# Performance work log

Measured on AMD Instinct MI355X. Metric: run time of the kernel, lower is better.

Reference implementation:

```python
import jax, jax.numpy as jnp
import numpy as np
from math import factorial, sqrt

LMAX = 2
NB = 32
NRBF = 20
CUTOFF = 5.0
N_ATOMS = 20000
N_EDGES = 400000
T = 2
M = (LMAX + 1) ** 2
LIDX = np.repeat(np.arange(LMAX + 1), 2 * np.arange(LMAX + 1) + 1)  # l of each flat (l,m) index


def _cg_complex(j1, m1, j2, m2, j3, m3):
    # Racah formula for complex-SH Clebsch-Gordan coefficients
    if m3 != m1 + m2 or j3 < abs(j1 - j2) or j3 > j1 + j2:
        return 0.0
    f = factorial
    pref = sqrt((2 * j3 + 1) * f(j1 + j2 - j3) * f(j1 - j2 + j3) * f(-j1 + j2 + j3) / f(j1 + j2 + j3 + 1))
    pref *= sqrt(f(j1 + m1) * f(j1 - m1) * f(j2 + m2) * f(j2 - m2) * f(j3 + m3) * f(j3 - m3))
    kmin = max(0, j2 - j3 - m1, j1 + m2 - j3)
    kmax = min(j1 + j2 - j3, j1 - m1, j2 + m2)
    s = 0.0
    for k in range(kmin, kmax + 1):
        s += (-1) ** k / (f(k) * f(j1 + j2 - j3 - k) * f(j1 - m1 - k) * f(j2 + m2 - k) * f(j3 - j2 + m1 + k) * f(j3 - j1 - m2 + k))
    return pref * s


def _u_matrix(l):
    # real-SH = U @ complex-SH (rows: real m from -l..l, cols: complex m')
    U = np.zeros((2 * l + 1, 2 * l + 1), dtype=np.complex128)
    for m in range(-l, l + 1):
        if m == 0:
            U[l, l] = 1.0
        elif m > 0:
            U[l + m, l + m] = (-1) ** m / sqrt(2)
            U[l + m, l - m] = 1.0 / sqrt(2)
        else:
            mu = -m
            U[l + m, l + m] = 1j / sqrt(2)
            U[l + m, l - m] = -1j * (-1) ** mu / sqrt(2)
    return U


def _build_cg_rsh(lmax):
    # CG coefficients in the real-SH basis, parity invariant (odd l1+l2+l3 blocks zero)
    cg = np.zeros((M, M, M), dtype=np.float64)
    Us = [_u_matrix(l) for l in range(lmax + 1)]
    for l1 in range(lmax + 1):
        for l2 in range(lmax + 1):
            for l3 in range(lmax + 1):
                if (l1 + l2 + l3) % 2 == 1 or l3 < abs(l1 - l2) or l3 > l1 + l2:
                    continue
                Cc = np.zeros((2 * l1 + 1, 2 * l2 + 1, 2 * l3 + 1), dtype=np.complex128)
                for i, m1 in enumerate(range(-l1, l1 + 1)):
                    for j, m2 in enumerate(range(-l2, l2 + 1)):
                        m3 = m1 + m2
                        if abs(m3) <= l3:
                            Cc[i, j, l3 + m3] = _cg_complex(l1, m1, l2, m2, l3, m3)
                R = np.einsum('ai,bj,ck,ijk->abc', Us[l1], Us[l2], np.conj(Us[l3]), Cc)
                cg[l1 * l1:(l1 + 1) ** 2, l2 * l2:(l2 + 1) ** 2, l3 * l3:(l3 + 1) ** 2] = np.real(R)
    return cg.astype(np.float32)


CG = jnp.asarray(_build_cg_rsh(LMAX))   # [9, 9, 9]
LIDX_J = jnp.asarray(LIDX)


def _rsh(dirs):
    # real spherical harmonics up to l=2 on unit vectors, flat (l,m) order -> [P, 9]
    x, y, z = dirs[:, 0], dirs[:, 1], dirs[:, 2]
    c1 = 0.4886025119029199
    c2 = 1.0925484305920792
    return jnp.stack([
        jnp.full_like(x, 0.28209479177387814),
        c1 * y, c1 * z, c1 * x,
        c2 * x * y, c2 * y * z,
        0.31539156525252005 * (3.0 * z * z - 1.0),
        c2 * x * z,
        0.5462742152960396 * (x * x - y * y),
    ], axis=1)


def _forward(atomic_numbers, r_ij, idx_i, idx_j, emb, Wf, bf, Wm1, Wm2, Wm3, Wg, bg):
    d = jnp.linalg.norm(r_ij, axis=1)                      # [P]
    Y = _rsh(r_ij / d[:, None])                            # [P, 9]
    offsets = jnp.linspace(0.0, CUTOFF, NRBF)
    width = CUTOFF / (NRBF - 1)
    radial = jnp.exp(-0.5 / width ** 2 * (d[:, None] - offsets) ** 2)   # GaussianRBF [P, NRBF]
    fcut = jnp.where(d < CUTOFF, 0.5 * (jnp.cos(d * jnp.pi / CUTOFF) + 1.0), 0.0)  # CosineCutoff
    x0 = emb[atomic_numbers]                               # nuclear embedding [N, NB]
    x = jnp.concatenate([x0[:, None, :], jnp.zeros((x0.shape[0], M - 1, NB), x0.dtype)], axis=1)  # scalar2rsh
    for t in range(T):
        # SO3Convolution: per-edge radial filter per output degree l, cutoff gated
        Wl = ((radial @ Wf[t].T + bf[t]) * fcut[:, None]).reshape(-1, LMAX + 1, NB)
        xj = x[idx_j]                                      # gather neighbors [P, 9, NB]
        tbc = jnp.einsum('pa,abc->pbc', Y, CG)             # contract Y_ij with CG
        yij = jnp.einsum('pbc,pbn->pcn', tbc, xj) * Wl[:, LIDX_J, :]
        dx = jax.ops.segment_sum(yij, idx_i, num_segments=x.shape[0], indices_are_sorted=True)
        ddx = jnp.einsum('xcn,kn->xck', dx, Wm1[t])        # mixing1 (no bias)
        dx = dx + jnp.einsum('abc,xan,xbn->xcn', CG, dx, ddx)  # SO3TensorProduct
        dx = jnp.einsum('xcn,kn->xck', dx, Wm2[t])         # mixing2
        h = jax.nn.sigmoid((dx[:, 0, :] @ Wg[t].T + bg[t]).reshape(-1, LMAX + 1, NB))
        dx = dx * h[:, LIDX_J, :]                          # SO3ParametricGatedNonlinearity
        dx = jnp.einsum('xcn,kn->xck', dx, Wm3[t])         # mixing3
        x = x + dx
    return x                                               # multipole representation [N, 9, NB]


def setup_inputs():
    key = jax.random.key(0)
    ks = jax.random.split(key, 12)
    return {
        'atomic_numbers': jax.random.randint(ks[0], (N_ATOMS,), 1, 100),
        'r_ij': jax.random.normal(ks[1], (N_EDGES, 3), jnp.float32),
        'idx_i': jnp.sort(jax.random.randint(ks[2], (N_EDGES,), 0, N_ATOMS)),
        'idx_j': jax.random.randint(ks[3], (N_EDGES,), 0, N_ATOMS),
        'emb': jax.random.normal(ks[4], (101, NB), jnp.float32).at[0].set(0.0),
        'Wf': jax.random.normal(ks[5], (T, (LMAX + 1) * NB, NRBF), jnp.float32) / sqrt(NRBF),
        'bf': jnp.zeros((T, (LMAX + 1) * NB), jnp.float32),
        'Wm1': jax.random.normal(ks[6], (T, NB, NB), jnp.float32) / sqrt(NB),
        'Wm2': jax.random.normal(ks[7], (T, NB, NB), jnp.float32) / sqrt(NB),
        'Wm3': jax.random.normal(ks[8], (T, NB, NB), jnp.float32) / sqrt(NB),
        'Wg': jax.random.normal(ks[9], (T, (LMAX + 1) * NB, NB), jnp.float32) / sqrt(NB),
        'bg': jnp.zeros((T, (LMAX + 1) * NB), jnp.float32),
    }


def reference(atomic_numbers, r_ij, idx_i, idx_j, emb, Wf, bf, Wm1, Wm2, Wm3, Wg, bg):
    return _forward(atomic_numbers, r_ij, idx_i, idx_j, emb, Wf, bf, Wm1, Wm2, Wm3, Wg, bg)
```

## Files before the change

### kernel.cpp

```cpp
#include <hip/hip_runtime.h>

#define CHUNK 16

constexpr double CFACT[8] = {1.,1.,2.,6.,24.,120.,720.,5040.};

constexpr double csqrt(double x){
  if (x <= 0.0) return 0.0;
  double s = 1.0;
  while (x > 4.0)  { x *= 0.25; s *= 2.0; }
  while (x < 0.25) { x *= 4.0;  s *= 0.5; }
  double g = 1.0;
  for (int i=0;i<10;i++) g = 0.5*(g + x/g);
  return s*g;
}

constexpr double cg_complex(int j1,int m1,int j2,int m2,int j3,int m3){
  if (m3 != m1+m2 || j3 < (j1>j2?j1-j2:j2-j1) || j3 > j1+j2) return 0.0;
  double pref = csqrt((2.0*j3+1.0)*CFACT[j1+j2-j3]*CFACT[j1-j2+j3]*CFACT[-j1+j2+j3]/CFACT[j1+j2+j3+1]);
  pref *= csqrt(CFACT[j1+m1]*CFACT[j1-m1]*CFACT[j2+m2]*CFACT[j2-m2]*CFACT[j3+m3]*CFACT[j3-m3]);
  int kmin = 0;
  if (j2-j3-m1 > kmin) kmin = j2-j3-m1;
  if (j1+m2-j3 > kmin) kmin = j1+m2-j3;
  int kmax = j1+j2-j3;
  if (j1-m1 < kmax) kmax = j1-m1;
  if (j2+m2 < kmax) kmax = j2+m2;
  double s = 0.0;
  for (int k=kmin;k<=kmax;++k){
    double t = 1.0/(CFACT[k]*CFACT[j1+j2-j3-k]*CFACT[j1-m1-k]*CFACT[j2+m2-k]*CFACT[j3-j2+m1+k]*CFACT[j3-j1-m2+k]);
    s += (k&1)? -t : t;
  }
  return pref*s;
}

struct UR { int n; int mc[2]; double re[2]; double im[2]; };
constexpr UR u_row(int m){
  UR u{}; const double is2 = 0.70710678118654752440;
  if (m==0){ u.n=1; u.mc[0]=0; u.re[0]=1.0; u.im[0]=0.0; u.mc[1]=0; u.re[1]=0.0; u.im[1]=0.0; }
  else if (m>0){ u.n=2; u.mc[0]=m;  u.re[0]=((m&1)? -is2:is2); u.im[0]=0.0;
                        u.mc[1]=-m; u.re[1]=is2;               u.im[1]=0.0; }
  else { int mu=-m; u.n=2; u.mc[0]=m;  u.re[0]=0.0; u.im[0]=is2;
                           u.mc[1]=mu; u.re[1]=0.0; u.im[1]=((mu&1)? is2:-is2); }
  return u;
}

struct CGTab { float v[9][9][9]; };
constexpr CGTab build_cg(){
  CGTab g{};
  double cc[9][9][9] = {};
  for (int a=0;a<9;a++){
    int l1 = (a==0)?0:((a<4)?1:2); int m1 = a - (l1*l1+l1);
    for (int b=0;b<9;b++){
      int l2 = (b==0)?0:((b<4)?1:2); int m2 = b - (l2*l2+l2);
      int m3 = m1+m2;
      for (int l3=0;l3<=2;l3++){
        if (m3 < -l3 || m3 > l3) continue;
        cc[a][b][l3*l3+l3+m3] = cg_complex(l1,m1,l2,m2,l3,m3);
      }
    }
  }
  for (int l1=0;l1<=2;l1++) for (int l2=0;l2<=2;l2++) for (int l3=0;l3<=2;l3++){
    if (((l1+l2+l3)&1)==1) continue;
    int dl = (l1>l2)?(l1-l2):(l2-l1);
    if (l3 < dl || l3 > l1+l2) continue;
    for (int m1=-l1;m1<=l1;m1++) for (int m2=-l2;m2<=l2;m2++) for (int m3=-l3;m3<=l3;m3++){
      UR ua = u_row(m1), ub = u_row(m2), uc = u_row(m3);
      double acc = 0.0;
      for (int i=0;i<ua.n;i++) for (int j=0;j<ub.n;j++){
        double zr = ua.re[i]*ub.re[j] - ua.im[i]*ub.im[j];
        double zi = ua.re[i]*ub.im[j] + ua.im[i]*ub.re[j];
        for (int k=0;k<uc.n;k++){
          double rp = zr*uc.re[k] + zi*uc.im[k];
          if (rp != 0.0)
            acc += rp * cc[l1*l1+l1+ua.mc[i]][l2*l2+l2+ub.mc[j]][l3*l3+l3+uc.mc[k]];
        }
      }
      g.v[l1*l1+l1+m1][l2*l2+l2+m2][l3*l3+l3+m3] = (float)acc;
    }
  }
  return g;
}
constexpr CGTab CGT = build_cg();

__global__ void init_x_kernel(const int* __restrict__ Z, const float* __restrict__ emb,
                              float4* __restrict__ x4, float4* __restrict__ dx4, int n_atoms){
  int i = blockIdx.x*blockDim.x + threadIdx.x;
  if (i >= n_atoms*72) return;
  int atom = i/72, rem = i - atom*72;
  float4 v = make_float4(0.f,0.f,0.f,0.f);
  if (rem < 8) v = reinterpret_cast<const float4*>(emb)[Z[atom]*8 + rem];
  x4[i] = v;
  dx4[i] = make_float4(0.f,0.f,0.f,0.f);
}

__global__ __launch_bounds__(256) void edge_kernel(
    const float* __restrict__ r_ij, const int* __restrict__ idx_i, const int* __restrict__ idx_j,
    const float* __restrict__ x, const float* __restrict__ Wf_t, const float* __restrict__ bf_t,
    float* __restrict__ dx, int n_edges)
{
  int tid = threadIdx.x;
  int g = tid >> 5, lane = tid & 31;

  int base = (blockIdx.x*8 + g)*CHUNK;
  if (base >= n_edges) return;

  int pidx;
  {
    int e0 = base + (lane & 15);
    if (e0 > n_edges-1) e0 = n_edges-1;
    pidx = (lane < 16) ? idx_i[e0] : idx_j[e0];
  }
  float rv0, rv1;
  {
    long long rmax = (long long)n_edges*3 - 1;
    long long a0 = (long long)base*3 + lane;       if (a0 > rmax) a0 = rmax;
    long long a1 = (long long)base*3 + 32 + lane;  if (a1 > rmax) a1 = rmax;
    rv0 = r_ij[a0];
    rv1 = r_ij[a1];
  }

  float wfr[3][20]; float bfl[3];
  #pragma unroll
  for (int l=0;l<3;l++){
    const float* rp = Wf_t + (l*32+lane)*20;
    #pragma unroll
    for (int q=0;q<5;q++){
      float4 v4 = *reinterpret_cast<const float4*>(rp + q*4);
      wfr[l][q*4+0]=v4.x; wfr[l][q*4+1]=v4.y; wfr[l][q*4+2]=v4.z; wfr[l][q*4+3]=v4.w;
    }
    bfl[l] = bf_t[l*32+lane];
  }

  const float STEP  = 5.0f/19.0f;
  const float ALPHA = -0.5f/(STEP*STEP);
  float myoff = (float)lane * STEP;

  float racc[9];
  #pragma unroll
  for (int c=0;c<9;c++) racc[c]=0.f;
  int cur_i = -1;

  float xjn[9];
  {
    int j0 = __shfl(pidx, 16, 32);
    const float* xp = x + j0*288 + lane;
    #pragma unroll
    for (int b=0;b<9;b++) xjn[b] = xp[b*32];
  }

  #pragma unroll
  for (int k=0;k<CHUNK;k++){
    int e = base + k;
    if (e >= n_edges) break;

    float xj[9];
    #pragma unroll
    for (int b=0;b<9;b++) xj[b] = xjn[b];

    if (k+1 < CHUNK){
      int jn = __shfl(pidx, 16+k+1, 32);
      const float* xp = x + jn*288 + lane;
      #pragma unroll
      for (int b=0;b<9;b++) xjn[b] = xp[b*32];
    }

    int ii = __shfl(pidx, k, 32);

    float rx = (3*k+0 < 32) ? __shfl(rv0, 3*k+0, 32) : __shfl(rv1, 3*k+0-32, 32);
    float ry = (3*k+1 < 32) ? __shfl(rv0, 3*k+1, 32) : __shfl(rv1, 3*k+1-32, 32);
    float rz = (3*k+2 < 32) ? __shfl(rv0, 3*k+2, 32) : __shfl(rv1, 3*k+2-32, 32);

    float d2 = fmaf(rx,rx,fmaf(ry,ry,rz*rz));
    float dd = sqrtf(d2);
    float inv = __fdividef(1.0f, dd);
    float X = rx*inv, Yv = ry*inv, Zv = rz*inv;
    const float c1 = 0.4886025119029199f, c2 = 1.0925484305920792f;
    float Y[9];
    Y[0]=0.28209479177387814f; Y[1]=c1*Yv; Y[2]=c1*Zv; Y[3]=c1*X;
    Y[4]=c2*X*Yv; Y[5]=c2*Yv*Zv; Y[6]=0.31539156525252005f*(3.f*Zv*Zv-1.f);
    Y[7]=c2*X*Zv; Y[8]=0.5462742152960396f*(X*X-Yv*Yv);

    float dtl = dd - myoff;
    float rbl = __expf(ALPHA*dtl*dtl);
    float wl0=bfl[0], wl1=bfl[1], wl2=bfl[2];
    #pragma unroll
    for (int r=0;r<20;r++){
      float rb = __shfl(rbl, r, 32);
      wl0 = fmaf(rb, wfr[0][r], wl0);
      wl1 = fmaf(rb, wfr[1][r], wl1);
      wl2 = fmaf(rb, wfr[2][r], wl2);
    }
    float fc = (dd < 5.0f) ? 0.5f*(__cosf(dd*0.6283185307179586f)+1.0f) : 0.0f;
    wl0*=fc; wl1*=fc; wl2*=fc;

    if (ii != cur_i){
      if (cur_i >= 0){
        float* dp = dx + cur_i*288 + lane;
        #pragma unroll
        for (int c=0;c<9;c++){ atomicAdd(dp + c*32, racc[c]); racc[c]=0.f; }
      }
      cur_i = ii;
    }

    float yv[9];
    #pragma unroll
    for (int c=0;c<9;c++) yv[c]=0.f;
    #pragma unroll
    for (int a=0;a<9;a++){
      #pragma unroll
      for (int b=0;b<9;b++){
        bool any = false;
        #pragma unroll
        for (int c=0;c<9;c++) any = any | (CGT.v[a][b][c] != 0.f);
        if (any){
          float p = Y[a]*xj[b];
          #pragma unroll
          for (int c=0;c<9;c++){
            if (CGT.v[a][b][c] != 0.f) yv[c] = fmaf(CGT.v[a][b][c], p, yv[c]);
          }
        }
      }
    }
    racc[0] = fmaf(wl0, yv[0], racc[0]);
    #pragma unroll
    for (int c=1;c<4;c++) racc[c] = fmaf(wl1, yv[c], racc[c]);
    #pragma unroll
    for (int c=4;c<9;c++) racc[c] = fmaf(wl2, yv[c], racc[c]);
  }
  if (cur_i >= 0){
    float* dp = dx + cur_i*288 + lane;
    #pragma unroll
    for (int c=0;c<9;c++) atomicAdd(dp + c*32, racc[c]);
  }
}

__global__ __launch_bounds__(256,4) void atom_kernel(
    float* __restrict__ x, float* __restrict__ dxg,
    const float* __restrict__ Wm1_t, const float* __restrict__ Wm2_t, const float* __restrict__ Wm3_t,
    const float* __restrict__ Wg_t, const float* __restrict__ bg_t, int n_atoms)
{
  __shared__ float W1T[1024], W2T[1024], W3T[1024];
  __shared__ float WgT[3072];
  __shared__ float bgs[96];
  __shared__ __align__(16) float tile[8][288];
  int tid = threadIdx.x;
  for (int i=tid;i<1024;i+=256){ int n=i>>5, kk=i&31; W1T[i]=Wm1_t[kk*32+n]; W2T[i]=Wm2_t[kk*32+n]; W3T[i]=Wm3_t[kk*32+n]; }
  for (int i=tid;i<3072;i+=256){ int n=i/96, jj=i-n*96; WgT[i]=Wg_t[jj*32+n]; }
  for (int i=tid;i<96;i+=256) bgs[i]=bg_t[i];
  __syncthreads();

  int g = tid>>5, k = tid&31;
  float* tg = &tile[g][0];
  const float4* t4 = reinterpret_cast<const float4*>(tg);

  float wr1[32], wr2[32], wr3[32];
  #pragma unroll
  for (int n=0;n<32;n++){ wr1[n]=W1T[n*32+k]; }

  for (int atom = blockIdx.x*8 + g; atom < n_atoms; atom += gridDim.x*8){
    float* dp = dxg + atom*288 + k;
    float v[9];
    #pragma unroll
    for (int c=0;c<9;c++){ v[c]=dp[c*32]; tg[c*32+k]=v[c]; dp[c*32]=0.f; }

    float u[9];
    #pragma unroll
    for (int c=0;c<9;c++){
      float s=0.f;
      #pragma unroll
      for (int q=0;q<8;q++){
        float4 tv = t4[c*8+q];
        s = fmaf(tv.x, wr1[4*q+0], s); s = fmaf(tv.y, wr1[4*q+1], s);
        s = fmaf(tv.z, wr1[4*q+2], s); s = fmaf(tv.w, wr1[4*q+3], s);
      }
      u[c]=s;
    }

    float w[9];
    #pragma unroll
    for (int c=0;c<9;c++) w[c]=v[c];
    #pragma unroll
    for (int a=0;a<9;a++){
      #pragma unroll
      for (int b=0;b<9;b++){
        bool any = false;
        #pragma unroll
        for (int c=0;c<9;c++) any = any | (CGT.v[a][b][c] != 0.f);
        if (any){
          float p = v[a]*u[b];
          #pragma unroll
          for (int c=0;c<9;c++){
            if (CGT.v[a][b][c] != 0.f) w[c] = fmaf(CGT.v[a][b][c], p, w[c]);
          }
        }
      }
    }

    #pragma unroll
    for (int c=0;c<9;c++) tg[c*32+k]=w[c];
    #pragma unroll
    for (int n=0;n<32;n++) wr2[n]=W2T[n*32+k];
    float p[9];
    #pragma unroll
    for (int c=0;c<9;c++){
      float s=0.f;
      #pragma unroll
      for (int q=0;q<8;q++){
        float4 tv = t4[c*8+q];
        s = fmaf(tv.x, wr2[4*q+0], s); s = fmaf(tv.y, wr2[4*q+1], s);
        s = fmaf(tv.z, wr2[4*q+2], s); s = fmaf(tv.w, wr2[4*q+3], s);
      }
      p[c]=s;
    }

    tg[k] = p[0];
    float s0=bgs[k], s1=bgs[32+k], s2=bgs[64+k];
    #pragma unroll
    for (int q=0;q<8;q++){
      float4 tv = t4[q];
      #pragma unroll
      for (int z=0;z<4;z++){
        float tvz = (z==0)?tv.x:((z==1)?tv.y:((z==2)?tv.z:tv.w));
        int n = 4*q+z;
        s0 = fmaf(tvz, WgT[n*96 + k],      s0);
        s1 = fmaf(tvz, WgT[n*96 + 32 + k], s1);
        s2 = fmaf(tvz, WgT[n*96 + 64 + k], s2);
      }
    }
    float h0 = 1.f/(1.f+__expf(-s0));
    float h1 = 1.f/(1.f+__expf(-s1));
    float h2 = 1.f/(1.f+__expf(-s2));

    float q9[9];
    q9[0]=p[0]*h0;
    #pragma unroll
    for (int c=1;c<4;c++) q9[c]=p[c]*h1;
    #pragma unroll
    for (int c=4;c<9;c++) q9[c]=p[c]*h2;

    #pragma unroll
    for (int c=0;c<9;c++) tg[c*32+k]=q9[c];
    #pragma unroll
    for (int n=0;n<32;n++) wr3[n]=W3T[n*32+k];
    float* xo = x + atom*288 + k;
    #pragma unroll
    for (int c=0;c<9;c++){
      float s=0.f;
      #pragma unroll
      for (int q=0;q<8;q++){
        float4 tv = t4[c*8+q];
        s = fmaf(tv.x, wr3[4*q+0], s); s = fmaf(tv.y, wr3[4*q+1], s);
        s = fmaf(tv.z, wr3[4*q+2], s); s = fmaf(tv.w, wr3[4*q+3], s);
      }
      xo[c*32] += s;
    }
  }
}

extern "C" void kernel_launch(void* const* d_in, const int* in_sizes, int n_in,
                              void* d_out, int out_size, void* d_ws, size_t ws_size,
                              hipStream_t stream)
{
  const int*   Z    = (const int*)d_in[0];
  const float* r_ij = (const float*)d_in[1];
  const int*   idxi = (const int*)d_in[2];
  const int*   idxj = (const int*)d_in[3];
  const float* emb  = (const float*)d_in[4];
  const float* Wf   = (const float*)d_in[5];
  const float* bf   = (const float*)d_in[6];
  const float* Wm1  = (const float*)d_in[7];
  const float* Wm2  = (const float*)d_in[8];
  const float* Wm3  = (const float*)d_in[9];
  const float* Wg   = (const float*)d_in[10];
  const float* bg   = (const float*)d_in[11];
  int n_atoms = in_sizes[0];
  int n_edges = in_sizes[1]/3;

  float* x  = (float*)d_out;
  float* dx = (float*)d_ws;

  init_x_kernel<<<(n_atoms*72+255)/256,256,0,stream>>>(Z, emb, (float4*)x, (float4*)dx, n_atoms);

  int ablocks = (n_atoms + 7)/8; if (ablocks > 640) ablocks = 640;
  for (int t=0;t<2;t++){
    int eblocks = (n_edges + 8*CHUNK - 1)/(8*CHUNK);
    edge_kernel<<<eblocks,256,0,stream>>>(r_ij, idxi, idxj, x,
                                          Wf + t*96*20, bf + t*96, dx, n_edges);
    atom_kernel<<<ablocks,256,0,stream>>>(x, dx,
                                          Wm1 + t*1024, Wm2 + t*1024, Wm3 + t*1024,
                                          Wg + t*96*32, bg + t*96, n_atoms);
  }
}
```

Measured before the change: 433.2 us.

## Specialize first edge pass for scalar-only features; simplify atom kernel weight loading

For the first interaction the node features are known to be nonzero only in the l=0 channel (from embedding init), so a templated edge kernel gathers just one value per neighbor and replaces the full Clebsch-Gordan contraction with a direct Y*x0 product. The atom kernel drops the shared-memory transposed weight staging and grid-stride loop, launching one warp per atom and reading weights row-wise from global memory as float4. This cuts gather traffic and FMA work in the first edge pass, but relies on the structural zero of higher-l channels after init. The atom kernel loses weight reuse across atoms and leans on cache hits for weight reads.

```diff
diff --git a/kernel.cpp b/kernel.cpp
--- a/kernel.cpp
+++ b/kernel.cpp
@@ -92,6 +92,7 @@
   dx4[i] = make_float4(0.f,0.f,0.f,0.f);
 }
 
+template<bool FIRST>
 __global__ __launch_bounds__(256) void edge_kernel(
     const float* __restrict__ r_ij, const int* __restrict__ idx_i, const int* __restrict__ idx_j,
     const float* __restrict__ x, const float* __restrict__ Wf_t, const float* __restrict__ bf_t,
@@ -140,11 +141,16 @@
   int cur_i = -1;
 
   float xjn[9];
+  float xjn0;
   {
     int j0 = __shfl(pidx, 16, 32);
     const float* xp = x + j0*288 + lane;
-    #pragma unroll
-    for (int b=0;b<9;b++) xjn[b] = xp[b*32];
+    if (FIRST){
+      xjn0 = xp[0];
+    } else {
+      #pragma unroll
+      for (int b=0;b<9;b++) xjn[b] = xp[b*32];
+    }
   }
 
   #pragma unroll
@@ -152,15 +158,23 @@
     int e = base + k;
     if (e >= n_edges) break;
 
-    float xj[9];
-    #pragma unroll
-    for (int b=0;b<9;b++) xj[b] = xjn[b];
+    float xj[9]; float xj0;
+    if (FIRST){
+      xj0 = xjn0;
+    } else {
+      #pragma unroll
+      for (int b=0;b<9;b++) xj[b] = xjn[b];
+    }
 
     if (k+1 < CHUNK){
       int jn = __shfl(pidx, 16+k+1, 32);
       const float* xp = x + jn*288 + lane;
-      #pragma unroll
-      for (int b=0;b<9;b++) xjn[b] = xp[b*32];
+      if (FIRST){
+        xjn0 = xp[0];
+      } else {
+        #pragma unroll
+        for (int b=0;b<9;b++) xjn[b] = xp[b*32];
+      }
     }
 
     int ii = __shfl(pidx, k, 32);
@@ -201,30 +215,38 @@
       cur_i = ii;
     }
 
-    float yv[9];
-    #pragma unroll
-    for (int c=0;c<9;c++) yv[c]=0.f;
-    #pragma unroll
-    for (int a=0;a<9;a++){
-      #pragma unroll
-      for (int b=0;b<9;b++){
-        bool any = false;
+    if (FIRST){
+      racc[0] = fmaf(wl0, Y[0]*xj0, racc[0]);
+      #pragma unroll
+      for (int c=1;c<4;c++) racc[c] = fmaf(wl1, Y[c]*xj0, racc[c]);
+      #pragma unroll
+      for (int c=4;c<9;c++) racc[c] = fmaf(wl2, Y[c]*xj0, racc[c]);
+    } else {
+      float yv[9];
+      #pragma unroll
+      for (int c=0;c<9;c++) yv[c]=0.f;
+      #pragma unroll
+      for (int a=0;a<9;a++){
         #pragma unroll
-        for (int c=0;c<9;c++) any = any | (CGT.v[a][b][c] != 0.f);
-        if (any){
-          float p = Y[a]*xj[b];
+        for (int b=0;b<9;b++){
+          bool any = false;
           #pragma unroll
-          for (int c=0;c<9;c++){
-            if (CGT.v[a][b][c] != 0.f) yv[c] = fmaf(CGT.v[a][b][c], p, yv[c]);
+          for (int c=0;c<9;c++) any = any | (CGT.v[a][b][c] != 0.f);
+          if (any){
+            float p = Y[a]*xj[b];
+            #pragma unroll
+            for (int c=0;c<9;c++){
+              if (CGT.v[a][b][c] != 0.f) yv[c] = fmaf(CGT.v[a][b][c], p, yv[c]);
+            }
           }
         }
       }
-    }
-    racc[0] = fmaf(wl0, yv[0], racc[0]);
-    #pragma unroll
-    for (int c=1;c<4;c++) racc[c] = fmaf(wl1, yv[c], racc[c]);
-    #pragma unroll
-    for (int c=4;c<9;c++) racc[c] = fmaf(wl2, yv[c], racc[c]);
+      racc[0] = fmaf(wl0, yv[0], racc[0]);
+      #pragma unroll
+      for (int c=1;c<4;c++) racc[c] = fmaf(wl1, yv[c], racc[c]);
+      #pragma unroll
+      for (int c=4;c<9;c++) racc[c] = fmaf(wl2, yv[c], racc[c]);
+    }
   }
   if (cur_i >= 0){
     float* dp = dx + cur_i*288 + lane;
@@ -233,126 +255,127 @@
   }
 }
 
-__global__ __launch_bounds__(256,4) void atom_kernel(
+__global__ __launch_bounds__(256) void atom_kernel(
     float* __restrict__ x, float* __restrict__ dxg,
     const float* __restrict__ Wm1_t, const float* __restrict__ Wm2_t, const float* __restrict__ Wm3_t,
     const float* __restrict__ Wg_t, const float* __restrict__ bg_t, int n_atoms)
 {
-  __shared__ float W1T[1024], W2T[1024], W3T[1024];
-  __shared__ float WgT[3072];
-  __shared__ float bgs[96];
   __shared__ __align__(16) float tile[8][288];
   int tid = threadIdx.x;
-  for (int i=tid;i<1024;i+=256){ int n=i>>5, kk=i&31; W1T[i]=Wm1_t[kk*32+n]; W2T[i]=Wm2_t[kk*32+n]; W3T[i]=Wm3_t[kk*32+n]; }
-  for (int i=tid;i<3072;i+=256){ int n=i/96, jj=i-n*96; WgT[i]=Wg_t[jj*32+n]; }
-  for (int i=tid;i<96;i+=256) bgs[i]=bg_t[i];
-  __syncthreads();
-
   int g = tid>>5, k = tid&31;
+  int atom = blockIdx.x*8 + g;
+  if (atom >= n_atoms) return;
   float* tg = &tile[g][0];
   const float4* t4 = reinterpret_cast<const float4*>(tg);
 
-  float wr1[32], wr2[32], wr3[32];
-  #pragma unroll
-  for (int n=0;n<32;n++){ wr1[n]=W1T[n*32+k]; }
-
-  for (int atom = blockIdx.x*8 + g; atom < n_atoms; atom += gridDim.x*8){
-    float* dp = dxg + atom*288 + k;
-    float v[9];
-    #pragma unroll
-    for (int c=0;c<9;c++){ v[c]=dp[c*32]; tg[c*32+k]=v[c]; dp[c*32]=0.f; }
-
-    float u[9];
-    #pragma unroll
-    for (int c=0;c<9;c++){
-      float s=0.f;
-      #pragma unroll
-      for (int q=0;q<8;q++){
-        float4 tv = t4[c*8+q];
-        s = fmaf(tv.x, wr1[4*q+0], s); s = fmaf(tv.y, wr1[4*q+1], s);
-        s = fmaf(tv.z, wr1[4*q+2], s); s = fmaf(tv.w, wr1[4*q+3], s);
-      }
-      u[c]=s;
-    }
-
-    float w[9];
-    #pragma unroll
-    for (int c=0;c<9;c++) w[c]=v[c];
-    #pragma unroll
-    for (int a=0;a<9;a++){
-      #pragma unroll
-      for (int b=0;b<9;b++){
-        bool any = false;
+  float* dp = dxg + atom*288 + k;
+  float v[9];
+  #pragma unroll
+  for (int c=0;c<9;c++){ v[c]=dp[c*32]; tg[c*32+k]=v[c]; dp[c*32]=0.f; }
+
+  float wr[32];
+  {
+    const float4* w4 = reinterpret_cast<const float4*>(Wm1_t + k*32);
+    #pragma unroll
+    for (int q=0;q<8;q++){ float4 a=w4[q]; wr[4*q]=a.x; wr[4*q+1]=a.y; wr[4*q+2]=a.z; wr[4*q+3]=a.w; }
+  }
+  float u[9];
+  #pragma unroll
+  for (int c=0;c<9;c++){
+    float s=0.f;
+    #pragma unroll
+    for (int q=0;q<8;q++){
+      float4 tv = t4[c*8+q];
+      s = fmaf(tv.x, wr[4*q+0], s); s = fmaf(tv.y, wr[4*q+1], s);
+      s = fmaf(tv.z, wr[4*q+2], s); s = fmaf(tv.w, wr[4*q+3], s);
+    }
+    u[c]=s;
+  }
+
+  float w[9];
+  #pragma unroll
+  for (int c=0;c<9;c++) w[c]=v[c];
+  #pragma unroll
+  for (int a=0;a<9;a++){
+    #pragma unroll
+    for (int b=0;b<9;b++){
+      bool any = false;
+      #pragma unroll
+      for (int c=0;c<9;c++) any = any | (CGT.v[a][b][c] != 0.f);
+      if (any){
+        float p = v[a]*u[b];
         #pragma unroll
-        for (int c=0;c<9;c++) any = any | (CGT.v[a][b][c] != 0.f);
-        if (any){
-          float p = v[a]*u[b];
-          #pragma unroll
-          for (int c=0;c<9;c++){
-            if (CGT.v[a][b][c] != 0.f) w[c] = fmaf(CGT.v[a][b][c], p, w[c]);
-          }
+        for (int c=0;c<9;c++){
+          if (CGT.v[a][b][c] != 0.f) w[c] = fmaf(CGT.v[a][b][c], p, w[c]);
         }
       }
     }
-
-    #pragma unroll
-    for (int c=0;c<9;c++) tg[c*32+k]=w[c];
-    #pragma unroll
-    for (int n=0;n<32;n++) wr2[n]=W2T[n*32+k];
-    float p[9];
-    #pragma unroll
-    for (int c=0;c<9;c++){
-      float s=0.f;
-      #pragma unroll
-      for (int q=0;q<8;q++){
-        float4 tv = t4[c*8+q];
-        s = fmaf(tv.x, wr2[4*q+0], s); s = fmaf(tv.y, wr2[4*q+1], s);
-        s = fmaf(tv.z, wr2[4*q+2], s); s = fmaf(tv.w, wr2[4*q+3], s);
-      }
-      p[c]=s;
-    }
-
-    tg[k] = p[0];
-    float s0=bgs[k], s1=bgs[32+k], s2=bgs[64+k];
+  }
+
+  #pragma unroll
+  for (int c=0;c<9;c++) tg[c*32+k]=w[c];
+  {
+    const float4* w4 = reinterpret_cast<const float4*>(Wm2_t + k*32);
+    #pragma unroll
+    for (int q=0;q<8;q++){ float4 a=w4[q]; wr[4*q]=a.x; wr[4*q+1]=a.y; wr[4*q+2]=a.z; wr[4*q+3]=a.w; }
+  }
+  float p[9];
+  #pragma unroll
+  for (int c=0;c<9;c++){
+    float s=0.f;
+    #pragma unroll
+    for (int q=0;q<8;q++){
+      float4 tv = t4[c*8+q];
+      s = fmaf(tv.x, wr[4*q+0], s); s = fmaf(tv.y, wr[4*q+1], s);
+      s = fmaf(tv.z, wr[4*q+2], s); s = fmaf(tv.w, wr[4*q+3], s);
+    }
+    p[c]=s;
+  }
+
+  tg[k] = p[0];
+  float s0=bg_t[k], s1=bg_t[32+k], s2=bg_t[64+k];
+  {
+    const float4* wg0 = reinterpret_cast<const float4*>(Wg_t + (     k)*32);
+    const float4* wg1 = reinterpret_cast<const float4*>(Wg_t + (32 + k)*32);
+    const float4* wg2 = reinterpret_cast<const float4*>(Wg_t + (64 + k)*32);
     #pragma unroll
     for (int q=0;q<8;q++){
       float4 tv = t4[q];
-      #pragma unroll
-      for (int z=0;z<4;z++){
-        float tvz = (z==0)?tv.x:((z==1)?tv.y:((z==2)?tv.z:tv.w));
-        int n = 4*q+z;
-        s0 = fmaf(tvz, WgT[n*96 + k],      s0);
-        s1 = fmaf(tvz, WgT[n*96 + 32 + k], s1);
-        s2 = fmaf(tvz, WgT[n*96 + 64 + k], s2);
-      }
-    }
-    float h0 = 1.f/(1.f+__expf(-s0));
-    float h1 = 1.f/(1.f+__expf(-s1));
-    float h2 = 1.f/(1.f+__expf(-s2));
-
-    float q9[9];
-    q9[0]=p[0]*h0;
-    #pragma unroll
-    for (int c=1;c<4;c++) q9[c]=p[c]*h1;
-    #pragma unroll
-    for (int c=4;c<9;c++) q9[c]=p[c]*h2;
-
-    #pragma unroll
-    for (int c=0;c<9;c++) tg[c*32+k]=q9[c];
-    #pragma unroll
-    for (int n=0;n<32;n++) wr3[n]=W3T[n*32+k];
-    float* xo = x + atom*288 + k;
-    #pragma unroll
-    for (int c=0;c<9;c++){
-      float s=0.f;
-      #pragma unroll
-      for (int q=0;q<8;q++){
-        float4 tv = t4[c*8+q];
-        s = fmaf(tv.x, wr3[4*q+0], s); s = fmaf(tv.y, wr3[4*q+1], s);
-        s = fmaf(tv.z, wr3[4*q+2], s); s = fmaf(tv.w, wr3[4*q+3], s);
-      }
-      xo[c*32] += s;
-    }
+      float4 a0 = wg0[q], a1 = wg1[q], a2 = wg2[q];
+      s0 = fmaf(tv.x,a0.x,s0); s0 = fmaf(tv.y,a0.y,s0); s0 = fmaf(tv.z,a0.z,s0); s0 = fmaf(tv.w,a0.w,s0);
+      s1 = fmaf(tv.x,a1.x,s1); s1 = fmaf(tv.y,a1.y,s1); s1 = fmaf(tv.z,a1.z,s1); s1 = fmaf(tv.w,a1.w,s1);
+      s2 = fmaf(tv.x,a2.x,s2); s2 = fmaf(tv.y,a2.y,s2); s2 = fmaf(tv.z,a2.z,s2); s2 = fmaf(tv.w,a2.w,s2);
+    }
+  }
+  float h0 = 1.f/(1.f+__expf(-s0));
+  float h1 = 1.f/(1.f+__expf(-s1));
+  float h2 = 1.f/(1.f+__expf(-s2));
+
+  float q9[9];
+  q9[0]=p[0]*h0;
+  #pragma unroll
+  for (int c=1;c<4;c++) q9[c]=p[c]*h1;
+  #pragma unroll
+  for (int c=4;c<9;c++) q9[c]=p[c]*h2;
+
+  #pragma unroll
+  for (int c=0;c<9;c++) tg[c*32+k]=q9[c];
+  {
+    const float4* w4 = reinterpret_cast<const float4*>(Wm3_t + k*32);
+    #pragma unroll
+    for (int q=0;q<8;q++){ float4 a=w4[q]; wr[4*q]=a.x; wr[4*q+1]=a.y; wr[4*q+2]=a.z; wr[4*q+3]=a.w; }
+  }
+  float* xo = x + atom*288 + k;
+  #pragma unroll
+  for (int c=0;c<9;c++){
+    float s=0.f;
+    #pragma unroll
+    for (int q=0;q<8;q++){
+      float4 tv = t4[c*8+q];
+      s = fmaf(tv.x, wr[4*q+0], s); s = fmaf(tv.y, wr[4*q+1], s);
+      s = fmaf(tv.z, wr[4*q+2], s); s = fmaf(tv.w, wr[4*q+3], s);
+    }
+    xo[c*32] += s;
   }
 }
 
@@ -380,13 +403,15 @@
 
   init_x_kernel<<<(n_atoms*72+255)/256,256,0,stream>>>(Z, emb, (float4*)x, (float4*)dx, n_atoms);
 
-  int ablocks = (n_atoms + 7)/8; if (ablocks > 640) ablocks = 640;
-  for (int t=0;t<2;t++){
-    int eblocks = (n_edges + 8*CHUNK - 1)/(8*CHUNK);
-    edge_kernel<<<eblocks,256,0,stream>>>(r_ij, idxi, idxj, x,
-                                          Wf + t*96*20, bf + t*96, dx, n_edges);
-    atom_kernel<<<ablocks,256,0,stream>>>(x, dx,
-                                          Wm1 + t*1024, Wm2 + t*1024, Wm3 + t*1024,
-                                          Wg + t*96*32, bg + t*96, n_atoms);
-  }
-}
+  int eblocks = (n_edges + 8*CHUNK - 1)/(8*CHUNK);
+  int ablocks = (n_atoms + 7)/8;
+
+  edge_kernel<true><<<eblocks,256,0,stream>>>(r_ij, idxi, idxj, x, Wf, bf, dx, n_edges);
+  atom_kernel<<<ablocks,256,0,stream>>>(x, dx, Wm1, Wm2, Wm3, Wg, bg, n_atoms);
+
+  edge_kernel<false><<<eblocks,256,0,stream>>>(r_ij, idxi, idxj, x,
+                                        Wf + 96*20, bf + 96, dx, n_edges);
+  atom_kernel<<<ablocks,256,0,stream>>>(x, dx,
+                                        Wm1 + 1024, Wm2 + 1024, Wm3 + 1024,
+                                        Wg + 96*32, bg + 96, n_atoms);
+}
```

After: 414.8 us. 1.04x faster.
